# Kernel optimization log

Hardware: AMD Instinct MI355X
Metric: run time of the kernel (lower is better)

## Reference

```python
import jax, jax.numpy as jnp
import numpy as np

HEADS = 16


def setup_inputs() -> dict:
    key = jax.random.key(0)
    ks = jax.random.split(key, 7)
    B, N, MEM, DIM = 2, 2048, 2048, 1024
    J = MEM + N
    x = jax.random.normal(ks[0], (B, N, DIM), dtype=jnp.float32)
    mem = jax.random.normal(ks[1], (B, MEM, DIM), dtype=jnp.float32)
    expire_mask = jax.random.uniform(ks[2], (B, 1, 1, J), dtype=jnp.float32)
    Wq = jax.random.normal(ks[3], (DIM, DIM), dtype=jnp.float32) * 0.02
    Wkv = jax.random.normal(ks[4], (DIM, 2 * DIM), dtype=jnp.float32) * 0.02
    Wo = jax.random.normal(ks[5], (DIM, DIM), dtype=jnp.float32) * 0.02
    bo = jnp.zeros((DIM,), dtype=jnp.float32)
    return {"x": x, "mem": mem, "expire_mask": expire_mask,
            "Wq": Wq, "Wkv": Wkv, "Wo": Wo, "bo": bo}


def reference(x, mem, expire_mask, Wq, Wkv, Wo, bo):
    b, n, dim = x.shape
    h = HEADS
    d = dim // h
    scale = d ** -0.5
    mem_len = mem.shape[1]

    q = x @ Wq                                   # [b, n, dim]
    context = jnp.concatenate([mem, x], axis=1)  # [b, j, dim]
    kv = context @ Wkv                           # [b, j, 2*dim]
    k, v = jnp.split(kv, 2, axis=-1)

    def to_heads(t):
        bb, nn, _ = t.shape
        return t.reshape(bb, nn, h, d).transpose(0, 2, 1, 3)  # b h n d

    q, k, v = map(to_heads, (q, k, v))

    dots = jnp.einsum('bhid,bhjd->bhij', q, k) * scale  # [b,h,n,j]
    j_len = dots.shape[-1]
    # causal mask with memory offset: position i attends to j <= i + mem_len
    i_idx = jnp.arange(n)[:, None]
    j_idx = jnp.arange(j_len)[None, :]
    causal = j_idx > (i_idx + mem_len)           # True => masked
    dots = jnp.where(causal[None, None], -jnp.inf, dots)

    attn = jax.nn.softmax(dots, axis=-1)
    attn = attn * expire_mask                    # post-softmax expire gating

    out = jnp.einsum('bhij,bhjd->bhid', attn, v)  # [b,h,n,d]
    out = out.transpose(0, 2, 1, 3).reshape(b, n, dim)
    return out @ Wo + bo
```

## Files before the change

kernel.cpp:

```cpp
#include <hip/hip_runtime.h>
#include <cstdint>

typedef __bf16 bf16_t;
typedef __attribute__((ext_vector_type(2))) __bf16 bf16x2;
typedef __attribute__((ext_vector_type(4))) __bf16 bf16x4;
typedef __attribute__((ext_vector_type(8))) __bf16 bf16x8;
typedef __attribute__((ext_vector_type(4))) float f32x4;
typedef __attribute__((ext_vector_type(16))) float f32x16;
typedef __attribute__((ext_vector_type(4))) int i32x4;

constexpr int Bx = 2, Nx = 2048, MEMx = 2048, Jx = 4096, DIMx = 1024, Hx = 16, HDx = 64;

__device__ __forceinline__ void gload_lds16(const bf16_t* g, bf16_t* lds) {
  __builtin_amdgcn_global_load_lds(
      (const __attribute__((address_space(1))) unsigned int*)g,
      (__attribute__((address_space(3))) unsigned int*)lds, 16, 0, 0);
}

__device__ __forceinline__ int pk2(float a, float b) {
  bf16x2 t;
  t[0] = (bf16_t)a;
  t[1] = (bf16_t)b;
  return __builtin_bit_cast(int, t);
}

__device__ __forceinline__ void pl32swap(int& a, int& b) {
  asm volatile("v_permlane32_swap_b32 %0, %1" : "+v"(a), "+v"(b));
}

__device__ __forceinline__ float fmax3(float a, float b, float c) {
  float d;
  asm("v_max3_f32 %0, %1, %2, %3" : "=v"(d) : "v"(a), "v"(b), "v"(c));
  return d;
}

__global__ void k_build_bf16(const float* __restrict__ x, const float* __restrict__ mem,
                             bf16_t* __restrict__ xb, bf16_t* __restrict__ ctxb) {
  const int XT = Bx * Nx * DIMx;
  const int CT = Bx * Jx * DIMx;
  for (int i = blockIdx.x * blockDim.x + threadIdx.x; i < XT + CT;
       i += gridDim.x * blockDim.x) {
    if (i < XT) {
      xb[i] = (bf16_t)x[i];
    } else {
      int c = i - XT;
      int bb = c / (Jx * DIMx);
      int rr = c % (Jx * DIMx);
      int j = rr / DIMx, d = rr % DIMx;
      float v = (j < MEMx) ? mem[(int64_t)(bb * MEMx + j) * DIMx + d]
                           : x[(int64_t)(bb * Nx + (j - MEMx)) * DIMx + d];
      ctxb[c] = (bf16_t)v;
    }
  }
}

__global__ void k_transpose_w(const float* __restrict__ W, bf16_t* __restrict__ WT,
                              int K, int Nc) {
  int total = K * Nc;
  for (int i = blockIdx.x * blockDim.x + threadIdx.x; i < total;
       i += gridDim.x * blockDim.x) {
    int n = i / K, k = i % K;
    WT[i] = (bf16_t)W[(int64_t)k * Nc + n];
  }
}

template <int OUTF32>
__launch_bounds__(256)
__global__ void k_gemm_bt(const bf16_t* __restrict__ A, const bf16_t* __restrict__ BT,
                          void* __restrict__ Cv, const float* __restrict__ bias,
                          const float* __restrict__ gate, int gate_col0, float scale,
                          int M, int Nc, int K) {
  __shared__ bf16_t As[2][128 * 32];
  __shared__ bf16_t Bs[2][128 * 32];
  const int tid = threadIdx.x;
  const int w = tid >> 6, l = tid & 63;
  const int lr = l & 15, lg = l >> 4;
  const int m0 = blockIdx.y * 128, n0 = blockIdx.x * 128;
  const int wm = (w >> 1) * 64, wn = (w & 1) * 64;

  const int srow = w * 16 + (l >> 2);
  const int scol = (l & 3) * 8;
  const bf16_t* ga0 = A + (int64_t)(m0 + srow) * K + scol;
  const bf16_t* gb0 = BT + (int64_t)(n0 + srow) * K + scol;

  auto stage = [&](int bufi, int k0) {
    bf16_t* lA = &As[bufi][0] + w * 512;
    bf16_t* lB = &Bs[bufi][0] + w * 512;
    gload_lds16(ga0 + k0, lA);
    gload_lds16(ga0 + (int64_t)64 * K + k0, lA + 2048);
    gload_lds16(gb0 + k0, lB);
    gload_lds16(gb0 + (int64_t)64 * K + k0, lB + 2048);
  };

  f32x4 acc[4][4] = {};

  stage(0, 0);
  __syncthreads();

  const int nsteps = K >> 5;
  for (int t = 0; t < nsteps; ++t) {
    const int cur = t & 1;
    if (t + 1 < nsteps) stage(cur ^ 1, (t + 1) << 5);

    bf16x8 af[4], bfr[4];
#pragma unroll
    for (int q = 0; q < 4; ++q)
      af[q] = *(const bf16x8*)(&As[cur][0] + (wm + q * 16 + lr) * 32 + lg * 8);
#pragma unroll
    for (int q = 0; q < 4; ++q)
      bfr[q] = *(const bf16x8*)(&Bs[cur][0] + (wn + q * 16 + lr) * 32 + lg * 8);
#pragma unroll
    for (int mt = 0; mt < 4; ++mt)
#pragma unroll
      for (int nt = 0; nt < 4; ++nt)
        acc[mt][nt] = __builtin_amdgcn_mfma_f32_16x16x32_bf16(af[mt], bfr[nt],
                                                              acc[mt][nt], 0, 0, 0);
    __syncthreads();
  }

#pragma unroll
  for (int mt = 0; mt < 4; ++mt) {
#pragma unroll
    for (int nt = 0; nt < 4; ++nt) {
      int col = n0 + wn + nt * 16 + lr;
#pragma unroll
      for (int r = 0; r < 4; ++r) {
        int row = m0 + wm + mt * 16 + lg * 4 + r;
        float v = acc[mt][nt][r] * scale;
        if (gate != nullptr && col >= gate_col0) v *= gate[row];
        if constexpr (OUTF32) {
          ((float*)Cv)[(int64_t)row * Nc + col] = v + bias[col];
        } else {
          ((bf16_t*)Cv)[(int64_t)row * Nc + col] = (bf16_t)v;
        }
      }
    }
  }
}

__launch_bounds__(256)
__global__ void k_attn(const bf16_t* __restrict__ Q, const bf16_t* __restrict__ KV,
                       bf16_t* __restrict__ Opart, float2* __restrict__ ML) {
  __shared__ bf16_t Ks[2][64 * 64];
  __shared__ bf16_t Vs[2][64 * 80];

  const int tid = threadIdx.x;
  const int w = tid >> 6, l = tid & 63;
  const int ql = l & 31, hi = l >> 5;

  const int lin = blockIdx.x;
  const int qi0 = lin & 15, h = (lin >> 4) & 15;
  const int c = (lin >> 8) & 1, b = lin >> 9;
  const int qi = b ? (15 - qi0) : qi0;
  const int q0 = qi * 128;

  const bf16_t* Qb = Q + ((int64_t)b * Nx) * DIMx + h * HDx;
  const bf16_t* Kb = KV + ((int64_t)b * Jx) * (2 * DIMx) + h * HDx;
  const bf16_t* Vb = Kb + DIMx;

  const int qrow = q0 + w * 32 + ql;

  bf16x8 qf[4];
#pragma unroll
  for (int dt = 0; dt < 4; ++dt)
    qf[dt] = *(const bf16x8*)(Qb + (int64_t)qrow * DIMx + dt * 16 + hi * 8);

  int koff[2][4], voff[2][4];
#pragma unroll
  for (int jb = 0; jb < 2; ++jb)
#pragma unroll
    for (int dt = 0; dt < 4; ++dt)
      koff[jb][dt] = (jb * 32 + ql) * 128 + (((dt * 2 + hi) * 16) ^ ((ql & 7) * 16));
#pragma unroll
  for (int db = 0; db < 2; ++db)
#pragma unroll
    for (int jt = 0; jt < 4; ++jt)
      voff[db][jt] = (db * 32 + ql) * 160 +
                     (((jt * 2 + hi) * 16) ^ (((db * 4 + (ql >> 3)) & 7) * 16));

  f32x16 o[2] = {};
  float mrun = -1e30f, lsum = 0.f;

  const int ksrow = w * 16 + (l >> 3);
  const int kscol = ((l & 7) ^ (l >> 3)) * 8;
  const int jstart = c * 2048;
  const int jend = c ? ((Jx < q0 + 128 + MEMx) ? Jx : (q0 + 128 + MEMx)) : 2048;
  const int nt_tiles = (jend - jstart) >> 6;
  const f32x16 z16 = {};

  const bf16_t* vsrc0 = Vb + (int64_t)(w * 8 + (l >> 3)) * 2048 + (l & 7) * 8;
  const int vd0 = (l & 7) * 8;
  const int vrow2 = (l >> 3) * 2;
  const int chx0 = ((w) ^ (l & 7)) * 16;
  const int chx1 = ((4 + w) ^ (l & 7)) * 16;

  auto stageK = [&](int bufi, int j0) {
    bf16_t* kd = &Ks[bufi][0] + w * 1024;
    const bf16_t* src = Kb + (int64_t)(j0 + ksrow) * 2048 + kscol;
    gload_lds16(src, kd);
    gload_lds16(src + (int64_t)8 * 2048, kd + 512);
  };
  auto loadV = [&](int j0, bf16x8& a, bf16x8& cc) {
    const bf16_t* s = vsrc0 + (int64_t)j0 * 2048;
    a = *(const bf16x8*)s;
    cc = *(const bf16x8*)(s + (int64_t)32 * 2048);
  };
  auto writeV = [&](int bufi, bf16x8 a, bf16x8 cc) {
    char* base = (char*)&Vs[bufi][0];
#pragma unroll
    for (int i = 0; i < 8; ++i)
      *(bf16_t*)(base + (vd0 + i) * 160 + chx0 + vrow2) = a[i];
#pragma unroll
    for (int i = 0; i < 8; ++i)
      *(bf16_t*)(base + (vd0 + i) * 160 + chx1 + vrow2) = cc[i];
  };

  bf16x8 vA, vC;
  stageK(0, jstart);
  loadV(jstart, vA, vC);
  writeV(0, vA, vC);
  __syncthreads();

  for (int t = 0; t < nt_tiles; ++t) {
    const int cur = t & 1;
    const int j0 = jstart + (t << 6);
    const bool pf = (t + 1 < nt_tiles);
    if (pf) {
      stageK(cur ^ 1, j0 + 64);
      loadV(j0 + 64, vA, vC);
    }
    const char* KsC = (const char*)&Ks[cur][0];
    const char* VsC = (const char*)&Vs[cur][0];

    f32x16 s[2];
    __builtin_amdgcn_s_setprio(1);
#pragma unroll
    for (int jb = 0; jb < 2; ++jb) {
      f32x16 acc = z16;
#pragma unroll
      for (int dt = 0; dt < 4; ++dt) {
        bf16x8 kf = *(const bf16x8*)(KsC + koff[jb][dt]);
        acc = __builtin_amdgcn_mfma_f32_32x32x16_bf16(kf, qf[dt], acc, 0, 0, 0);
      }
      s[jb] = acc;
    }
    __builtin_amdgcn_s_setprio(0);

    if (j0 + 63 > q0 + MEMx) {
#pragma unroll
      for (int jb = 0; jb < 2; ++jb)
#pragma unroll
        for (int r = 0; r < 16; ++r) {
          int j = j0 + jb * 32 + (r & 3) + (r >> 2) * 8 + hi * 4;
          if (j > qrow + MEMx) s[jb][r] = -1e30f;
        }
    }

    float t12[12];
#pragma unroll
    for (int i = 0; i < 10; ++i)
      t12[i] = fmax3(s[(3 * i) >> 4][(3 * i) & 15], s[(3 * i + 1) >> 4][(3 * i + 1) & 15],
                     s[(3 * i + 2) >> 4][(3 * i + 2) & 15]);
    t12[10] = s[1][14];
    t12[11] = s[1][15];
    float t4[4];
#pragma unroll
    for (int i = 0; i < 4; ++i) t4[i] = fmax3(t12[3 * i], t12[3 * i + 1], t12[3 * i + 2]);
    float tm = fmaxf(fmax3(t4[0], t4[1], t4[2]), t4[3]);
    tm = fmaxf(tm, __shfl_xor(tm, 32));

    if (!__all(tm <= mrun + 8.f)) {
      float mnew = fmaxf(mrun, tm);
      float al = exp2f(mrun - mnew);
      mrun = mnew;
      lsum *= al;
#pragma unroll
      for (int db = 0; db < 2; ++db)
#pragma unroll
        for (int r = 0; r < 16; ++r) o[db][r] *= al;
    }

#pragma unroll
    for (int jb = 0; jb < 2; ++jb)
#pragma unroll
      for (int r = 0; r < 16; ++r) s[jb][r] = exp2f(s[jb][r] - mrun);

    f32x16 av = s[0] + s[1];
    float a8[8], a4[4];
#pragma unroll
    for (int i = 0; i < 8; ++i) a8[i] = av[i] + av[i + 8];
#pragma unroll
    for (int i = 0; i < 4; ++i) a4[i] = a8[i] + a8[i + 4];
    float ps = (a4[0] + a4[1]) + (a4[2] + a4[3]);
    ps += __shfl_xor(ps, 32);
    lsum += ps;

    bf16x8 pfrag[4];
#pragma unroll
    for (int jb = 0; jb < 2; ++jb) {
      int pw[8];
#pragma unroll
      for (int g = 0; g < 8; ++g) pw[g] = pk2(s[jb][2 * g], s[jb][2 * g + 1]);
      pl32swap(pw[0], pw[2]);
      pl32swap(pw[1], pw[3]);
      pl32swap(pw[4], pw[6]);
      pl32swap(pw[5], pw[7]);
      i32x4 f0 = {pw[0], pw[1], pw[2], pw[3]};
      i32x4 f1 = {pw[4], pw[5], pw[6], pw[7]};
      pfrag[jb * 2] = __builtin_bit_cast(bf16x8, f0);
      pfrag[jb * 2 + 1] = __builtin_bit_cast(bf16x8, f1);
    }

    __builtin_amdgcn_s_setprio(1);
#pragma unroll
    for (int db = 0; db < 2; ++db)
#pragma unroll
      for (int jt = 0; jt < 4; ++jt) {
        bf16x8 vf = *(const bf16x8*)(VsC + voff[db][jt]);
        o[db] = __builtin_amdgcn_mfma_f32_32x32x16_bf16(vf, pfrag[jt], o[db], 0, 0, 0);
      }
    __builtin_amdgcn_s_setprio(0);

    if (pf) writeV(cur ^ 1, vA, vC);
    __syncthreads();
  }

  bf16_t* op = Opart + (int64_t)c * (Bx * Nx * DIMx) +
               (int64_t)(b * Nx + qrow) * DIMx + h * HDx;
#pragma unroll
  for (int db = 0; db < 2; ++db)
#pragma unroll
    for (int g = 0; g < 4; ++g) {
      bf16x4 ov;
#pragma unroll
      for (int r = 0; r < 4; ++r) ov[r] = (bf16_t)o[db][g * 4 + r];
      *(bf16x4*)(op + db * 32 + g * 8 + hi * 4) = ov;
    }
  if (hi == 0)
    ML[((int64_t)(c * Bx + b) * Hx + h) * Nx + qrow] = make_float2(mrun, lsum);
}

__global__ void k_combine(const bf16_t* __restrict__ Op, const float2* __restrict__ ML,
                          bf16_t* __restrict__ Ho) {
  const int64_t CH = (int64_t)Bx * Nx * DIMx;
  int i = blockIdx.x * blockDim.x + threadIdx.x;
  const int total = (int)(CH >> 3);
  if (i >= total) return;
  int64_t off = (int64_t)i * 8;
  int bqh = (int)(off >> 6);
  int h = bqh & 15;
  int bq = bqh >> 4;
  int b = bq >> 11, q = bq & (Nx - 1);
  float2 ml0 = ML[((int64_t)b * Hx + h) * Nx + q];
  float2 ml1 = ML[((int64_t)(Bx + b) * Hx + h) * Nx + q];
  float M = fmaxf(ml0.x, ml1.x);
  float a0 = exp2f(ml0.x - M), a1 = exp2f(ml1.x - M);
  float inv = 1.f / (a0 * ml0.y + a1 * ml1.y);
  a0 *= inv;
  a1 *= inv;
  bf16x8 v0 = *(const bf16x8*)(Op + off);
  bf16x8 v1 = *(const bf16x8*)(Op + CH + off);
  bf16x8 outv;
#pragma unroll
  for (int r = 0; r < 8; ++r)
    outv[r] = (bf16_t)(a0 * (float)v0[r] + a1 * (float)v1[r]);
  *(bf16x8*)(Ho + off) = outv;
}

extern "C" void kernel_launch(void* const* d_in, const int* in_sizes, int n_in,
                              void* d_out, int out_size, void* d_ws, size_t ws_size,
                              hipStream_t stream) {
  const float* x    = (const float*)d_in[0];
  const float* mem  = (const float*)d_in[1];
  const float* expm = (const float*)d_in[2];
  const float* Wq   = (const float*)d_in[3];
  const float* Wkv  = (const float*)d_in[4];
  const float* Wo   = (const float*)d_in[5];
  const float* bo   = (const float*)d_in[6];
  float* out = (float*)d_out;

  bf16_t* p = (bf16_t*)d_ws;
  bf16_t* xb   = p; p += (size_t)Bx * Nx * DIMx;
  bf16_t* ctxb = p; p += (size_t)Bx * Jx * DIMx;
  bf16_t* WqT  = p; p += (size_t)DIMx * DIMx;
  bf16_t* WkvT = p; p += (size_t)DIMx * 2 * DIMx;
  bf16_t* WoT  = p; p += (size_t)DIMx * DIMx;
  bf16_t* Qb   = p; p += (size_t)Bx * Nx * DIMx;
  bf16_t* KVb  = p; p += (size_t)Bx * Jx * 2 * DIMx;
  bf16_t* Ho   = p; p += (size_t)Bx * Nx * DIMx;

  bf16_t* Opart = ctxb;
  float2* ML    = (float2*)xb;

  k_build_bf16<<<4096, 256, 0, stream>>>(x, mem, xb, ctxb);
  k_transpose_w<<<1024, 256, 0, stream>>>(Wq, WqT, DIMx, DIMx);
  k_transpose_w<<<2048, 256, 0, stream>>>(Wkv, WkvT, DIMx, 2 * DIMx);
  k_transpose_w<<<1024, 256, 0, stream>>>(Wo, WoT, DIMx, DIMx);

  const float qscale = 0.125f * 1.4426950408889634f;
  k_gemm_bt<0><<<dim3(1024 / 128, 4096 / 128), 256, 0, stream>>>(
      xb, WqT, Qb, nullptr, nullptr, 0x7fffffff, qscale, Bx * Nx, DIMx, DIMx);
  k_gemm_bt<0><<<dim3(2048 / 128, 8192 / 128), 256, 0, stream>>>(
      ctxb, WkvT, KVb, nullptr, expm, DIMx, 1.0f, Bx * Jx, 2 * DIMx, DIMx);

  k_attn<<<1024, 256, 0, stream>>>(Qb, KVb, Opart, ML);
  k_combine<<<(Bx * Nx * DIMx / 8 + 255) / 256, 256, 0, stream>>>(Opart, ML, Ho);

  k_gemm_bt<1><<<dim3(1024 / 128, 4096 / 128), 256, 0, stream>>>(
      Ho, WoT, out, bo, nullptr, 0x7fffffff, 1.0f, Bx * Nx, DIMx, DIMx);
}
```

Baseline: 301.0 us.

## Write V transposed from KV GEMM epilogue and async-stage K/V in attention

The KV projection GEMM now writes K into a compact buffer and writes V, already gated by the expire mask, in a per-head transposed layout [b,h,d,j]. This lets the attention kernel load V tiles straight into LDS with global_load_lds, the same way as K, instead of doing register loads followed by scattered 2-byte LDS writes. The attention loop becomes a deeper prefetch pipeline (two tiles in flight, explicit vmcnt waits and raw barriers). The cost is strided 8-byte stores in the GEMM epilogue for the transposed V, plus hand-written waitcnt synchronisation that has to be kept correct.

```diff
diff --git a/kernel.cpp b/kernel.cpp
--- a/kernel.cpp
+++ b/kernel.cpp
@@ -64,12 +64,12 @@
   }
 }
 
-template <int OUTF32>
+template <int MODE>
 __launch_bounds__(256)
 __global__ void k_gemm_bt(const bf16_t* __restrict__ A, const bf16_t* __restrict__ BT,
                           void* __restrict__ Cv, const float* __restrict__ bias,
-                          const float* __restrict__ gate, int gate_col0, float scale,
-                          int M, int Nc, int K) {
+                          const float* __restrict__ gate, bf16_t* __restrict__ VT,
+                          float scale, int M, int Nc, int K) {
   __shared__ bf16_t As[2][128 * 32];
   __shared__ bf16_t Bs[2][128 * 32];
   const int tid = threadIdx.x;
@@ -123,15 +123,29 @@
 #pragma unroll
     for (int nt = 0; nt < 4; ++nt) {
       int col = n0 + wn + nt * 16 + lr;
-#pragma unroll
-      for (int r = 0; r < 4; ++r) {
-        int row = m0 + wm + mt * 16 + lg * 4 + r;
-        float v = acc[mt][nt][r] * scale;
-        if (gate != nullptr && col >= gate_col0) v *= gate[row];
-        if constexpr (OUTF32) {
-          ((float*)Cv)[(int64_t)row * Nc + col] = v + bias[col];
+      int row0 = m0 + wm + mt * 16 + lg * 4;
+      if constexpr (MODE == 0) {
+#pragma unroll
+        for (int r = 0; r < 4; ++r)
+          ((bf16_t*)Cv)[(int64_t)(row0 + r) * Nc + col] =
+              (bf16_t)(acc[mt][nt][r] * scale);
+      } else if constexpr (MODE == 1) {
+#pragma unroll
+        for (int r = 0; r < 4; ++r)
+          ((float*)Cv)[(int64_t)(row0 + r) * Nc + col] = acc[mt][nt][r] + bias[col];
+      } else {
+        if (col < 1024) {
+#pragma unroll
+          for (int r = 0; r < 4; ++r)
+            ((bf16_t*)Cv)[(int64_t)(row0 + r) * 1024 + col] = (bf16_t)acc[mt][nt][r];
         } else {
-          ((bf16_t*)Cv)[(int64_t)row * Nc + col] = (bf16_t)v;
+          int hh = (col - 1024) >> 6, dd = col & 63;
+          int bb = row0 >> 12, jj = row0 & (Jx - 1);
+          bf16x4 ov;
+#pragma unroll
+          for (int r = 0; r < 4; ++r)
+            ov[r] = (bf16_t)(acc[mt][nt][r] * gate[row0 + r]);
+          *(bf16x4*)(VT + (((int64_t)(bb * Hx + hh) * HDx + dd) << 12) + jj) = ov;
         }
       }
     }
@@ -139,10 +153,11 @@
 }
 
 __launch_bounds__(256)
-__global__ void k_attn(const bf16_t* __restrict__ Q, const bf16_t* __restrict__ KV,
-                       bf16_t* __restrict__ Opart, float2* __restrict__ ML) {
+__global__ void k_attn(const bf16_t* __restrict__ Q, const bf16_t* __restrict__ Kbuf,
+                       const bf16_t* __restrict__ VT, bf16_t* __restrict__ Opart,
+                       float2* __restrict__ ML) {
   __shared__ bf16_t Ks[2][64 * 64];
-  __shared__ bf16_t Vs[2][64 * 80];
+  __shared__ bf16_t Vs[2][64 * 64];
 
   const int tid = threadIdx.x;
   const int w = tid >> 6, l = tid & 63;
@@ -155,8 +170,8 @@
   const int q0 = qi * 128;
 
   const bf16_t* Qb = Q + ((int64_t)b * Nx) * DIMx + h * HDx;
-  const bf16_t* Kb = KV + ((int64_t)b * Jx) * (2 * DIMx) + h * HDx;
-  const bf16_t* Vb = Kb + DIMx;
+  const bf16_t* Kb = Kbuf + ((int64_t)b * Jx) * 1024 + h * HDx;
+  const bf16_t* Vb = VT + ((int64_t)(b * Hx + h) * HDx << 12);
 
   const int qrow = q0 + w * 32 + ql;
 
@@ -164,6 +179,7 @@
 #pragma unroll
   for (int dt = 0; dt < 4; ++dt)
     qf[dt] = *(const bf16x8*)(Qb + (int64_t)qrow * DIMx + dt * 16 + hi * 8);
+  asm volatile("s_waitcnt vmcnt(0)" ::: "memory");
 
   int koff[2][4], voff[2][4];
 #pragma unroll
@@ -175,60 +191,45 @@
   for (int db = 0; db < 2; ++db)
 #pragma unroll
     for (int jt = 0; jt < 4; ++jt)
-      voff[db][jt] = (db * 32 + ql) * 160 +
-                     (((jt * 2 + hi) * 16) ^ (((db * 4 + (ql >> 3)) & 7) * 16));
+      voff[db][jt] = (db * 32 + ql) * 128 + (((jt * 2 + hi) * 16) ^ ((ql & 7) * 16));
 
   f32x16 o[2] = {};
   float mrun = -1e30f, lsum = 0.f;
 
-  const int ksrow = w * 16 + (l >> 3);
-  const int kscol = ((l & 7) ^ (l >> 3)) * 8;
+  const int srow8 = l >> 3;
+  const int swcol = ((l & 7) ^ srow8) * 8;
   const int jstart = c * 2048;
   const int jend = c ? ((Jx < q0 + 128 + MEMx) ? Jx : (q0 + 128 + MEMx)) : 2048;
   const int nt_tiles = (jend - jstart) >> 6;
   const f32x16 z16 = {};
 
-  const bf16_t* vsrc0 = Vb + (int64_t)(w * 8 + (l >> 3)) * 2048 + (l & 7) * 8;
-  const int vd0 = (l & 7) * 8;
-  const int vrow2 = (l >> 3) * 2;
-  const int chx0 = ((w) ^ (l & 7)) * 16;
-  const int chx1 = ((4 + w) ^ (l & 7)) * 16;
-
-  auto stageK = [&](int bufi, int j0) {
+  const bf16_t* ksrc0 = Kb + (int64_t)(w * 16 + srow8) * 1024 + swcol;
+  const bf16_t* vsrc0 = Vb + (int64_t)(w * 16 + srow8) * Jx + swcol;
+
+  auto stage = [&](int bufi, int j0) {
     bf16_t* kd = &Ks[bufi][0] + w * 1024;
-    const bf16_t* src = Kb + (int64_t)(j0 + ksrow) * 2048 + kscol;
-    gload_lds16(src, kd);
-    gload_lds16(src + (int64_t)8 * 2048, kd + 512);
+    const bf16_t* ks = ksrc0 + (int64_t)j0 * 1024;
+    gload_lds16(ks, kd);
+    gload_lds16(ks + 8 * 1024, kd + 512);
+    bf16_t* vd = &Vs[bufi][0] + w * 1024;
+    const bf16_t* vs = vsrc0 + j0;
+    gload_lds16(vs, vd);
+    gload_lds16(vs + 8 * Jx, vd + 512);
   };
-  auto loadV = [&](int j0, bf16x8& a, bf16x8& cc) {
-    const bf16_t* s = vsrc0 + (int64_t)j0 * 2048;
-    a = *(const bf16x8*)s;
-    cc = *(const bf16x8*)(s + (int64_t)32 * 2048);
-  };
-  auto writeV = [&](int bufi, bf16x8 a, bf16x8 cc) {
-    char* base = (char*)&Vs[bufi][0];
-#pragma unroll
-    for (int i = 0; i < 8; ++i)
-      *(bf16_t*)(base + (vd0 + i) * 160 + chx0 + vrow2) = a[i];
-#pragma unroll
-    for (int i = 0; i < 8; ++i)
-      *(bf16_t*)(base + (vd0 + i) * 160 + chx1 + vrow2) = cc[i];
-  };
-
-  bf16x8 vA, vC;
-  stageK(0, jstart);
-  loadV(jstart, vA, vC);
-  writeV(0, vA, vC);
-  __syncthreads();
+
+  stage(0, jstart);
+  stage(1, jstart + 64);
 
   for (int t = 0; t < nt_tiles; ++t) {
     const int cur = t & 1;
     const int j0 = jstart + (t << 6);
-    const bool pf = (t + 1 < nt_tiles);
-    if (pf) {
-      stageK(cur ^ 1, j0 + 64);
-      loadV(j0 + 64, vA, vC);
-    }
+    if (t + 1 < nt_tiles)
+      asm volatile("s_waitcnt vmcnt(4)" ::: "memory");
+    else
+      asm volatile("s_waitcnt vmcnt(0)" ::: "memory");
+    __builtin_amdgcn_s_barrier();
+    __builtin_amdgcn_sched_barrier(0);
+
     const char* KsC = (const char*)&Ks[cur][0];
     const char* VsC = (const char*)&Vs[cur][0];
 
@@ -321,8 +322,9 @@
       }
     __builtin_amdgcn_s_setprio(0);
 
-    if (pf) writeV(cur ^ 1, vA, vC);
-    __syncthreads();
+    __builtin_amdgcn_s_barrier();
+    __builtin_amdgcn_sched_barrier(0);
+    if (t + 2 < nt_tiles) stage(cur, jstart + ((t + 2) << 6));
   }
 
   bf16_t* op = Opart + (int64_t)c * (Bx * Nx * DIMx) +
@@ -389,6 +391,8 @@
   bf16_t* KVb  = p; p += (size_t)Bx * Jx * 2 * DIMx;
   bf16_t* Ho   = p; p += (size_t)Bx * Nx * DIMx;
 
+  bf16_t* Kbuf = KVb;
+  bf16_t* VT   = KVb + (size_t)Bx * Jx * 1024;
   bf16_t* Opart = ctxb;
   float2* ML    = (float2*)xb;
 
@@ -399,13 +403,13 @@
 
   const float qscale = 0.125f * 1.4426950408889634f;
   k_gemm_bt<0><<<dim3(1024 / 128, 4096 / 128), 256, 0, stream>>>(
-      xb, WqT, Qb, nullptr, nullptr, 0x7fffffff, qscale, Bx * Nx, DIMx, DIMx);
-  k_gemm_bt<0><<<dim3(2048 / 128, 8192 / 128), 256, 0, stream>>>(
-      ctxb, WkvT, KVb, nullptr, expm, DIMx, 1.0f, Bx * Jx, 2 * DIMx, DIMx);
-
-  k_attn<<<1024, 256, 0, stream>>>(Qb, KVb, Opart, ML);
+      xb, WqT, Qb, nullptr, nullptr, nullptr, qscale, Bx * Nx, DIMx, DIMx);
+  k_gemm_bt<2><<<dim3(2048 / 128, 8192 / 128), 256, 0, stream>>>(
+      ctxb, WkvT, Kbuf, nullptr, expm, VT, 1.0f, Bx * Jx, 2 * DIMx, DIMx);
+
+  k_attn<<<1024, 256, 0, stream>>>(Qb, Kbuf, VT, Opart, ML);
   k_combine<<<(Bx * Nx * DIMx / 8 + 255) / 256, 256, 0, stream>>>(Opart, ML, Ho);
 
   k_gemm_bt<1><<<dim3(1024 / 128, 4096 / 128), 256, 0, stream>>>(
-      Ho, WoT, out, bo, nullptr, 0x7fffffff, 1.0f, Bx * Nx, DIMx, DIMx);
-}
+      Ho, WoT, out, bo, nullptr, nullptr, 1.0f, Bx * Nx, DIMx, DIMx);
+}
```

Result: faster. 276.0 us (-8.3%).
